# Performance work log

Measured on AMD Instinct MI355X. Metric: run time of the kernel, lower is better.

## Reference

```python
import jax, jax.numpy as jnp
import numpy as np

B, S, D, E, TOP_K = 2, 1024, 1024, 8, 2
H = 4 * D  # FFN hidden


def setup_inputs() -> dict:
    key = jax.random.key(0)
    ks = jax.random.split(key, 12)
    sc = 0.02
    return {
        "x": jax.random.normal(ks[0], (B, S, D), jnp.float32),
        # gate: nn.Linear(D, E) -> weight [E, D], bias [E]; routing bias param [E]
        "Wg": jax.random.normal(ks[1], (E, D), jnp.float32) * sc,
        "bg": jnp.zeros((E,), jnp.float32),
        "bias": jnp.zeros((E,), jnp.float32),
        # routed experts: stacked Linear(D,4D) and Linear(4D,D) weights (torch layout [out,in])
        "W1": jax.random.normal(ks[2], (E, H, D), jnp.float32) * sc,
        "b1": jnp.zeros((E, H), jnp.float32),
        "W2": jax.random.normal(ks[3], (E, D, H), jnp.float32) * sc,
        "b2": jnp.zeros((E, D), jnp.float32),
        # shared expert
        "Ws1": jax.random.normal(ks[4], (H, D), jnp.float32) * sc,
        "bs1": jnp.zeros((H,), jnp.float32),
        "Ws2": jax.random.normal(ks[5], (D, H), jnp.float32) * sc,
        "bs2": jnp.zeros((D,), jnp.float32),
    }


def reference(x, Wg, bg, bias, W1, b1, W2, b2, Ws1, bs1, Ws2, bs2):
    b, s, d = x.shape
    xf = x.reshape(-1, d)  # [T, D]
    T = xf.shape[0]

    # sigmoid gating with learnable routing bias
    scores = jax.nn.sigmoid(xf @ Wg.T + bg + bias)          # [T, E]
    top_scores, top_idx = jax.lax.top_k(scores, TOP_K)      # [T, K]

    # per-token per-expert combine weights (zero for unselected experts)
    weights = jnp.zeros((T, E), scores.dtype)
    weights = weights.at[jnp.arange(T)[:, None], top_idx].add(top_scores)  # [T, E]

    # dense grouped expert MLP (mask-and-matmul form of gather-GEMM-scatter)
    h = jax.nn.gelu(jnp.einsum("td,ehd->teh", xf, W1) + b1, approximate=False)  # [T, E, H]
    eo = jnp.einsum("teh,edh->ted", h, W2) + b2                                  # [T, E, D]
    combined = jnp.einsum("ted,te->td", eo, weights)                             # [T, D]

    # shared expert applied to every token
    shared = jax.nn.gelu(xf @ Ws1.T + bs1, approximate=False) @ Ws2.T + bs2      # [T, D]

    return (shared + combined).reshape(b, s, d)
```

## Files before the change

kernel.cpp:

```cpp
#include <hip/hip_runtime.h>
#include <hip/hip_bf16.h>
#include <math.h>

#define NTOK 2048
#define DDIM 1024
#define HDIM 4096
#define NEXP 8
#define NROWS (3 * NTOK)
#define KSPLIT2 2

typedef __bf16 bf16x8 __attribute__((ext_vector_type(8)));
typedef float f32x4 __attribute__((ext_vector_type(4)));
typedef __attribute__((address_space(1))) char as1_char;
typedef __attribute__((address_space(3))) char as3_char;

__device__ __forceinline__ void async16(const void* g, void* l) {
  __builtin_amdgcn_global_load_lds((as1_char*)g, (as3_char*)l, 16, 0, 0);
}

__device__ __forceinline__ float gelu_fast(float v) {
  const float x = v * 0.70710678118654752f;
  const float ax = fabsf(x);
  const float t = __builtin_amdgcn_rcpf(1.0f + 0.3275911f * ax);
  float p = 1.061405429f;
  p = p * t - 1.453152027f;
  p = p * t + 1.421413741f;
  p = p * t - 0.284496736f;
  p = p * t + 0.254829592f;
  const float y = 1.0f - p * t * __expf(-ax * ax);
  const float erfv = copysignf(y, x);
  return 0.5f * v * (1.0f + erfv);
}

__global__ void moe_zero_misc(int* counts) {
  if (threadIdx.x < NEXP) counts[threadIdx.x] = 0;
}

__device__ __forceinline__ void cvt2048(const float* __restrict__ src,
                                        __hip_bfloat16* __restrict__ dst,
                                        int tid) {
  const size_t i = (size_t)tid * 8;
  const float4 a = *(const float4*)(src + i);
  const float4 b = *(const float4*)(src + i + 4);
  union { __hip_bfloat16 h[8]; uint4 u; } p;
  p.h[0] = __float2bfloat16(a.x); p.h[1] = __float2bfloat16(a.y);
  p.h[2] = __float2bfloat16(a.z); p.h[3] = __float2bfloat16(a.w);
  p.h[4] = __float2bfloat16(b.x); p.h[5] = __float2bfloat16(b.y);
  p.h[6] = __float2bfloat16(b.z); p.h[7] = __float2bfloat16(b.w);
  *(uint4*)(dst + i) = p.u;
}

__global__ void __launch_bounds__(256) moe_pre(
    const float* __restrict__ x, const float* __restrict__ Wg,
    const float* __restrict__ bg, const float* __restrict__ bias,
    const float* __restrict__ W1, const float* __restrict__ Ws1,
    __hip_bfloat16* __restrict__ xbf, __hip_bfloat16* __restrict__ W1bf,
    __hip_bfloat16* __restrict__ Ws1bf, float* __restrict__ out,
    int* __restrict__ counts, int* __restrict__ topk_idx,
    float* __restrict__ topk_w, int* __restrict__ slot) {
  const int b = blockIdx.x, tid = threadIdx.x;
  if (b < 512) {
    const int t = b * 4 + (tid >> 6);
    const int lane = tid & 63;
    float xv[16];
#pragma unroll
    for (int q = 0; q < 16; ++q) xv[q] = x[(size_t)t * DDIM + q * 64 + lane];
    float sc[NEXP];
#pragma unroll
    for (int e = 0; e < NEXP; ++e) {
      float s = 0.f;
#pragma unroll
      for (int q = 0; q < 16; ++q) s += xv[q] * Wg[(size_t)e * DDIM + q * 64 + lane];
#pragma unroll
      for (int o = 32; o > 0; o >>= 1) s += __shfl_xor(s, o, 64);
      sc[e] = 1.0f / (1.0f + expf(-(s + bg[e] + bias[e])));
    }
    if (lane == 0) {
      int k0 = 0;
      for (int e = 1; e < NEXP; ++e)
        if (sc[e] > sc[k0]) k0 = e;
      int k1 = (k0 == 0) ? 1 : 0;
      for (int e = 0; e < NEXP; ++e) {
        if (e == k0) continue;
        if (sc[e] > sc[k1]) k1 = e;
      }
      topk_idx[t * 2 + 0] = k0;
      topk_idx[t * 2 + 1] = k1;
      topk_w[t * 2 + 0] = sc[k0];
      topk_w[t * 2 + 1] = sc[k1];
      slot[t * 2 + 0] = atomicAdd(&counts[k0], 1);
      slot[t * 2 + 1] = atomicAdd(&counts[k1], 1);
    }
    return;
  }
  const int cb = b - 512;
  if (cb < 1024) { cvt2048(x + (size_t)cb * 2048, xbf + (size_t)cb * 2048, tid); return; }
  if (cb < 17408) { const size_t o = (size_t)(cb - 1024) * 2048; cvt2048(W1 + o, W1bf + o, tid); return; }
  if (cb < 19456) { const size_t o = (size_t)(cb - 17408) * 2048; cvt2048(Ws1 + o, Ws1bf + o, tid); return; }
  const size_t o = (size_t)(cb - 19456) * 2048 + (size_t)tid * 8;
  *(float4*)(out + o) = make_float4(0.f, 0.f, 0.f, 0.f);
  *(float4*)(out + o + 4) = make_float4(0.f, 0.f, 0.f, 0.f);
}

__device__ __forceinline__ void gemm_core(const char* ga0, const char* ga1,
                                          const char* gb0, const char* gb1,
                                          char* sm, int Kbytes, int tid,
                                          f32x4 acc[4][4]) {
  const int w = tid >> 6, l = tid & 63;
  const int lr = l & 15, quad = l >> 4;
  const int wr = w >> 1, wc = w & 1;
  const int swz = (lr >> 1) & 3;
  const int aoff = (wr * 64 + lr) * 64 + ((quad ^ swz) * 16);
  const int boff = 8192 + (wc * 64 + lr) * 64 + ((quad ^ swz) * 16);
  const int niter = Kbytes >> 6;

  auto stage = [&](int it, int buf) {
    char* base = sm + buf * 16384 + w * 1024;
    const int kb = it * 64;
    async16(ga0 + kb, base);
    async16(ga1 + kb, base + 4096);
    async16(gb0 + kb, base + 8192);
    async16(gb1 + kb, base + 12288);
  };

  stage(0, 0);
  __builtin_amdgcn_s_waitcnt(0x0F70);
  __builtin_amdgcn_s_barrier();
  for (int i = 0; i < niter; ++i) {
    const int cur = i & 1;
    const bool more = (i + 1 < niter);
    if (more) stage(i + 1, cur ^ 1);
    const char* rb = sm + cur * 16384;
    bf16x8 av[4], bv[4];
#pragma unroll
    for (int i2 = 0; i2 < 4; ++i2) av[i2] = *(const bf16x8*)(rb + aoff + i2 * 1024);
#pragma unroll
    for (int j = 0; j < 4; ++j) bv[j] = *(const bf16x8*)(rb + boff + j * 1024);
#pragma unroll
    for (int i2 = 0; i2 < 4; ++i2)
#pragma unroll
      for (int j = 0; j < 4; ++j)
        acc[i2][j] = __builtin_amdgcn_mfma_f32_16x16x32_bf16(av[i2], bv[j], acc[i2][j], 0, 0, 0);
    if (more) {
      __builtin_amdgcn_s_waitcnt(0x0F70);
      __builtin_amdgcn_s_barrier();
    }
  }
}

__device__ __forceinline__ int stage_colb(int l) {
  return (((l & 3) ^ ((l >> 3) & 3)) * 16);
}

__device__ __forceinline__ void xcd_decode(int hw, int& g, int& m) {
  m = (hw >> 3) & 7;
  g = (hw & 7) + 8 * (hw >> 6);
}

__global__ void moe_scan(const int* __restrict__ counts, int* __restrict__ offsets) {
  if (threadIdx.x == 0) {
    int s = 0;
    for (int e = 0; e < NEXP; ++e) { offsets[e] = s; s += counts[e]; }
    offsets[NEXP] = s;
  }
}

__global__ void moe_scatter(const int* __restrict__ topk_idx, const float* __restrict__ topk_w,
                            const int* __restrict__ slot, const int* __restrict__ offsets,
                            int* __restrict__ row_token, float* __restrict__ row_w) {
  const int t = blockIdx.x * blockDim.x + threadIdx.x;
  if (t >= NTOK) return;
#pragma unroll
  for (int k = 0; k < 2; ++k) {
    const int e = topk_idx[t * 2 + k];
    const int rg = offsets[e] + slot[t * 2 + k];
    row_token[rg] = t;
    row_w[rg] = topk_w[t * 2 + k];
  }
  row_token[2 * NTOK + t] = t;
  row_w[2 * NTOK + t] = 1.0f;
}

__device__ __forceinline__ void cvt_w2_quota(int b, const float* __restrict__ W2,
                                             const float* __restrict__ Ws2,
                                             __hip_bfloat16* __restrict__ W2bf,
                                             __hip_bfloat16* __restrict__ Ws2bf,
                                             int tid) {
  const float* src;
  __hip_bfloat16* dst;
  size_t base;
  if (b < 4096) { src = W2; dst = W2bf; base = (size_t)b * 8192; }
  else          { src = Ws2; dst = Ws2bf; base = (size_t)(b - 4096) * 8192; }
#pragma unroll
  for (int k = 0; k < 8; ++k) {
    const size_t i = base + (size_t)k * 1024 + (size_t)tid * 4;
    const float4 a = *(const float4*)(src + i);
    union { __hip_bfloat16 h[4]; uint2 u; } p;
    p.h[0] = __float2bfloat16(a.x); p.h[1] = __float2bfloat16(a.y);
    p.h[2] = __float2bfloat16(a.z); p.h[3] = __float2bfloat16(a.w);
    *(uint2*)(dst + i) = p.u;
  }
}

__global__ void __launch_bounds__(256) moe_gemm1(
    const __hip_bfloat16* __restrict__ xbf, const __hip_bfloat16* __restrict__ W1bf,
    const float* __restrict__ b1, const __hip_bfloat16* __restrict__ Ws1bf,
    const float* __restrict__ bs1, const int* __restrict__ counts,
    const int* __restrict__ offsets, const int* __restrict__ row_token,
    __hip_bfloat16* __restrict__ h1, const float* __restrict__ W2,
    const float* __restrict__ Ws2, __hip_bfloat16* __restrict__ W2bf,
    __hip_bfloat16* __restrict__ Ws2bf) {
  __shared__ alignas(16) char sm[32768];
  const int tid = threadIdx.x;
  int g, m;
  xcd_decode(blockIdx.x, g, m);
  const int nt = m + 8 * (g & 3);
  const int mt = (g >> 2) & 15;
  const int e = g >> 6;
  const int cnt = (e < NEXP) ? counts[e] : NTOK;
  if (mt * 128 >= cnt) {
    cvt_w2_quota(blockIdx.x, W2, Ws2, W2bf, Ws2bf, tid);
    return;
  }
  const int off = (e < NEXP) ? offsets[e] : 2 * NTOK;
  const __hip_bfloat16* Bw = (e < NEXP) ? (W1bf + (size_t)e * HDIM * DDIM) : Ws1bf;
  const float* bb = (e < NEXP) ? (b1 + e * HDIM) : bs1;

  const int w = tid >> 6, l = tid & 63;
  const int mrow = w * 16 + (l >> 2);
  const int colb = stage_colb(l);

  const int r0 = mt * 128 + mrow, r1 = r0 + 64;
  const int c0 = (r0 < cnt) ? r0 : (cnt - 1);
  const int c1 = (r1 < cnt) ? r1 : (cnt - 1);
  const int t0 = row_token[off + c0];
  const int t1 = row_token[off + c1];
  const char* ga0 = (const char*)xbf + (size_t)t0 * (DDIM * 2) + colb;
  const char* ga1 = (const char*)xbf + (size_t)t1 * (DDIM * 2) + colb;
  const char* gb0 = (const char*)Bw + (size_t)(nt * 128 + mrow) * (DDIM * 2) + colb;
  const char* gb1 = (const char*)Bw + (size_t)(nt * 128 + mrow + 64) * (DDIM * 2) + colb;

  f32x4 acc[4][4] = {};
  gemm_core(ga0, ga1, gb0, gb1, sm, DDIM * 2, tid, acc);

  const int lr = l & 15, quad = l >> 4, wr = w >> 1, wc = w & 1;
#pragma unroll
  for (int i = 0; i < 4; ++i) {
#pragma unroll
    for (int r = 0; r < 4; ++r) {
      const int rowe = mt * 128 + wr * 64 + i * 16 + quad * 4 + r;
      if (rowe >= cnt) continue;
      const size_t orow = (size_t)(off + rowe) * HDIM;
#pragma unroll
      for (int j = 0; j < 4; ++j) {
        const int h = nt * 128 + wc * 64 + j * 16 + lr;
        const float v = acc[i][j][r] + bb[h];
        h1[orow + h] = __float2bfloat16(gelu_fast(v));
      }
    }
  }
  cvt_w2_quota(blockIdx.x, W2, Ws2, W2bf, Ws2bf, tid);
}

__global__ void __launch_bounds__(256) moe_gemm2(
    const __hip_bfloat16* __restrict__ h1, const __hip_bfloat16* __restrict__ W2bf,
    const float* __restrict__ b2, const __hip_bfloat16* __restrict__ Ws2bf,
    const float* __restrict__ bs2, const int* __restrict__ counts,
    const int* __restrict__ offsets, const int* __restrict__ row_token,
    const float* __restrict__ row_w, float* __restrict__ out) {
  __shared__ alignas(16) char sm[32768];
  int g, m;
  xcd_decode(blockIdx.x, g, m);
  const int nt = m;
  const int kc = g & 1;
  const int mt = (g >> 1) & 15;
  const int e = g >> 5;
  const int cnt = (e < NEXP) ? counts[e] : NTOK;
  if (mt * 128 >= cnt) return;
  const int off = (e < NEXP) ? offsets[e] : 2 * NTOK;
  const __hip_bfloat16* Bw = (e < NEXP) ? (W2bf + (size_t)e * DDIM * HDIM) : Ws2bf;
  const float* bb = (e < NEXP) ? (b2 + e * DDIM) : bs2;

  const int tid = threadIdx.x;
  const int w = tid >> 6, l = tid & 63;
  const int mrow = w * 16 + (l >> 2);
  const int colb = stage_colb(l);
  const int KB = (HDIM * 2) / KSPLIT2;
  const size_t kofs = (size_t)kc * KB;

  const char* ga0 = (const char*)h1 + (size_t)(off + mt * 128 + mrow) * (HDIM * 2) + kofs + colb;
  const char* ga1 = (const char*)h1 + (size_t)(off + mt * 128 + mrow + 64) * (HDIM * 2) + kofs + colb;
  const char* gb0 = (const char*)Bw + (size_t)(nt * 128 + mrow) * (HDIM * 2) + kofs + colb;
  const char* gb1 = (const char*)Bw + (size_t)(nt * 128 + mrow + 64) * (HDIM * 2) + kofs + colb;

  f32x4 acc[4][4] = {};
  gemm_core(ga0, ga1, gb0, gb1, sm, KB, tid, acc);

  const int lr = l & 15, quad = l >> 4, wr = w >> 1, wc = w & 1;
#pragma unroll
  for (int i = 0; i < 4; ++i) {
#pragma unroll
    for (int r = 0; r < 4; ++r) {
      const int rowe = mt * 128 + wr * 64 + i * 16 + quad * 4 + r;
      if (rowe >= cnt) continue;
      const int rg = off + rowe;
      const int tok = row_token[rg];
      const float wt = row_w[rg];
#pragma unroll
      for (int j = 0; j < 4; ++j) {
        const int d = nt * 128 + wc * 64 + j * 16 + lr;
        const float base = (kc == 0) ? bb[d] : 0.f;
        atomicAdd(&out[(size_t)tok * DDIM + d], wt * (acc[i][j][r] + base));
      }
    }
  }
}

extern "C" void kernel_launch(void* const* d_in, const int* in_sizes, int n_in,
                              void* d_out, int out_size, void* d_ws, size_t ws_size,
                              hipStream_t stream) {
  (void)in_sizes; (void)n_in; (void)out_size; (void)ws_size;
  const float* x    = (const float*)d_in[0];
  const float* Wg   = (const float*)d_in[1];
  const float* bg   = (const float*)d_in[2];
  const float* bias = (const float*)d_in[3];
  const float* W1   = (const float*)d_in[4];
  const float* b1   = (const float*)d_in[5];
  const float* W2   = (const float*)d_in[6];
  const float* b2   = (const float*)d_in[7];
  const float* Ws1  = (const float*)d_in[8];
  const float* bs1  = (const float*)d_in[9];
  const float* Ws2  = (const float*)d_in[10];
  const float* bs2  = (const float*)d_in[11];
  float* out = (float*)d_out;

  char* ws = (char*)d_ws;
  size_t cur = 0;
  auto take = [&](size_t b) -> void* {
    void* p = ws + cur;
    cur += (b + 255) & ~(size_t)255;
    return p;
  };
  int* counts    = (int*)take(NEXP * 4);
  int* offsets   = (int*)take((NEXP + 1) * 4);
  int* topk_idx  = (int*)take(NTOK * 2 * 4);
  float* topk_w  = (float*)take(NTOK * 2 * 4);
  int* slot      = (int*)take(NTOK * 2 * 4);
  int* row_token = (int*)take(NROWS * 4);
  float* row_w   = (float*)take(NROWS * 4);
  __hip_bfloat16* xbf   = (__hip_bfloat16*)take((size_t)NTOK * DDIM * 2);
  __hip_bfloat16* W1bf  = (__hip_bfloat16*)take((size_t)NEXP * HDIM * DDIM * 2);
  __hip_bfloat16* W2bf  = (__hip_bfloat16*)take((size_t)NEXP * DDIM * HDIM * 2);
  __hip_bfloat16* Ws1bf = (__hip_bfloat16*)take((size_t)HDIM * DDIM * 2);
  __hip_bfloat16* Ws2bf = (__hip_bfloat16*)take((size_t)DDIM * HDIM * 2);
  __hip_bfloat16* h1    = (__hip_bfloat16*)take((size_t)(NROWS + 64) * HDIM * 2);

  moe_zero_misc<<<1, 64, 0, stream>>>(counts);

  moe_pre<<<20992, 256, 0, stream>>>(x, Wg, bg, bias, W1, Ws1,
                                     xbf, W1bf, Ws1bf, out,
                                     counts, topk_idx, topk_w, slot);

  moe_scan<<<1, 1, 0, stream>>>(counts, offsets);
  moe_scatter<<<NTOK / 256, 256, 0, stream>>>(topk_idx, topk_w, slot, offsets, row_token, row_w);

  moe_gemm1<<<4608, 256, 0, stream>>>(xbf, W1bf, b1, Ws1bf, bs1, counts, offsets,
                                      row_token, h1, W2, Ws2, W2bf, Ws2bf);

  moe_gemm2<<<2304, 256, 0, stream>>>(h1, W2bf, b2, Ws2bf, bs2, counts, offsets,
                                      row_token, row_w, out);
}
```

Baseline: 362.5 us.

## Double K-tile depth to 128 bytes with 8-way XOR swizzle and deeper prefetch

The shared GEMM core now stages a 64-element K slice per iteration instead of 32, using 64KB of LDS double buffering, an 8-slot XOR swizzle and four row pointers per operand. It waits only for the older batch of async loads (partial vmcnt) before the barrier, so the next tile's loads stay in flight during compute, and it issues twice as many MFMAs per barrier. The aim is to halve barrier and loop overhead and hide global-to-LDS latency better. The cost is doubled LDS per block, which may cut occupancy, plus an extra barrier per iteration.

Result: faster. 328.2 us (-9.5%).

```diff
diff --git a/kernel.cpp b/kernel.cpp
--- a/kernel.cpp
+++ b/kernel.cpp
@@ -102,54 +102,60 @@
   *(float4*)(out + o + 4) = make_float4(0.f, 0.f, 0.f, 0.f);
 }
 
-__device__ __forceinline__ void gemm_core(const char* ga0, const char* ga1,
-                                          const char* gb0, const char* gb1,
+__device__ __forceinline__ void gemm_core(const char* const ga[4], const char* const gb[4],
                                           char* sm, int Kbytes, int tid,
                                           f32x4 acc[4][4]) {
   const int w = tid >> 6, l = tid & 63;
   const int lr = l & 15, quad = l >> 4;
   const int wr = w >> 1, wc = w & 1;
-  const int swz = (lr >> 1) & 3;
-  const int aoff = (wr * 64 + lr) * 64 + ((quad ^ swz) * 16);
-  const int boff = 8192 + (wc * 64 + lr) * 64 + ((quad ^ swz) * 16);
-  const int niter = Kbytes >> 6;
+  const int s8 = lr & 7;
+  const int slot0 = (quad ^ s8) * 16;
+  const int slot1 = ((4 + quad) ^ s8) * 16;
+  const int abase = (wr * 64 + lr) * 128;
+  const int bbase = 16384 + (wc * 64 + lr) * 128;
+  const int niter = Kbytes >> 7;
 
   auto stage = [&](int it, int buf) {
-    char* base = sm + buf * 16384 + w * 1024;
-    const int kb = it * 64;
-    async16(ga0 + kb, base);
-    async16(ga1 + kb, base + 4096);
-    async16(gb0 + kb, base + 8192);
-    async16(gb1 + kb, base + 12288);
+    char* base = sm + buf * 32768;
+    const int kb = it * 128;
+#pragma unroll
+    for (int q = 0; q < 4; ++q) {
+      async16(ga[q] + kb, base + w * 4096 + q * 1024);
+      async16(gb[q] + kb, base + 16384 + w * 4096 + q * 1024);
+    }
   };
 
   stage(0, 0);
-  __builtin_amdgcn_s_waitcnt(0x0F70);
-  __builtin_amdgcn_s_barrier();
   for (int i = 0; i < niter; ++i) {
     const int cur = i & 1;
-    const bool more = (i + 1 < niter);
-    if (more) stage(i + 1, cur ^ 1);
-    const char* rb = sm + cur * 16384;
-    bf16x8 av[4], bv[4];
-#pragma unroll
-    for (int i2 = 0; i2 < 4; ++i2) av[i2] = *(const bf16x8*)(rb + aoff + i2 * 1024);
-#pragma unroll
-    for (int j = 0; j < 4; ++j) bv[j] = *(const bf16x8*)(rb + boff + j * 1024);
-#pragma unroll
-    for (int i2 = 0; i2 < 4; ++i2)
-#pragma unroll
-      for (int j = 0; j < 4; ++j)
-        acc[i2][j] = __builtin_amdgcn_mfma_f32_16x16x32_bf16(av[i2], bv[j], acc[i2][j], 0, 0, 0);
-    if (more) {
+    if (i + 1 < niter) {
+      stage(i + 1, cur ^ 1);
+      __builtin_amdgcn_s_waitcnt(0x0F78);
+    } else {
       __builtin_amdgcn_s_waitcnt(0x0F70);
-      __builtin_amdgcn_s_barrier();
-    }
-  }
-}
-
-__device__ __forceinline__ int stage_colb(int l) {
-  return (((l & 3) ^ ((l >> 3) & 3)) * 16);
+    }
+    __builtin_amdgcn_s_barrier();
+    const char* rb = sm + cur * 32768;
+    bf16x8 av[4][2], bv[4][2];
+#pragma unroll
+    for (int i2 = 0; i2 < 4; ++i2) {
+      av[i2][0] = *(const bf16x8*)(rb + abase + i2 * 2048 + slot0);
+      av[i2][1] = *(const bf16x8*)(rb + abase + i2 * 2048 + slot1);
+    }
+#pragma unroll
+    for (int j = 0; j < 4; ++j) {
+      bv[j][0] = *(const bf16x8*)(rb + bbase + j * 2048 + slot0);
+      bv[j][1] = *(const bf16x8*)(rb + bbase + j * 2048 + slot1);
+    }
+#pragma unroll
+    for (int s = 0; s < 2; ++s)
+#pragma unroll
+      for (int i2 = 0; i2 < 4; ++i2)
+#pragma unroll
+        for (int j = 0; j < 4; ++j)
+          acc[i2][j] = __builtin_amdgcn_mfma_f32_16x16x32_bf16(av[i2][s], bv[j][s], acc[i2][j], 0, 0, 0);
+    __builtin_amdgcn_s_barrier();
+  }
 }
 
 __device__ __forceinline__ void xcd_decode(int hw, int& g, int& m) {
@@ -210,7 +216,7 @@
     __hip_bfloat16* __restrict__ h1, const float* __restrict__ W2,
     const float* __restrict__ Ws2, __hip_bfloat16* __restrict__ W2bf,
     __hip_bfloat16* __restrict__ Ws2bf) {
-  __shared__ alignas(16) char sm[32768];
+  __shared__ alignas(16) char sm[65536];
   const int tid = threadIdx.x;
   int g, m;
   xcd_decode(blockIdx.x, g, m);
@@ -227,21 +233,22 @@
   const float* bb = (e < NEXP) ? (b1 + e * HDIM) : bs1;
 
   const int w = tid >> 6, l = tid & 63;
-  const int mrow = w * 16 + (l >> 2);
-  const int colb = stage_colb(l);
-
-  const int r0 = mt * 128 + mrow, r1 = r0 + 64;
-  const int c0 = (r0 < cnt) ? r0 : (cnt - 1);
-  const int c1 = (r1 < cnt) ? r1 : (cnt - 1);
-  const int t0 = row_token[off + c0];
-  const int t1 = row_token[off + c1];
-  const char* ga0 = (const char*)xbf + (size_t)t0 * (DDIM * 2) + colb;
-  const char* ga1 = (const char*)xbf + (size_t)t1 * (DDIM * 2) + colb;
-  const char* gb0 = (const char*)Bw + (size_t)(nt * 128 + mrow) * (DDIM * 2) + colb;
-  const char* gb1 = (const char*)Bw + (size_t)(nt * 128 + mrow + 64) * (DDIM * 2) + colb;
+  const int rl8 = l >> 3;
+  const int cg = ((l & 7) ^ rl8) * 16;
+
+  const char* ga[4];
+  const char* gb[4];
+#pragma unroll
+  for (int q = 0; q < 4; ++q) {
+    const int r = mt * 128 + w * 32 + q * 8 + rl8;
+    const int c = (r < cnt) ? r : (cnt - 1);
+    const int tok = row_token[off + c];
+    ga[q] = (const char*)xbf + (size_t)tok * (DDIM * 2) + cg;
+    gb[q] = (const char*)Bw + (size_t)(nt * 128 + w * 32 + q * 8 + rl8) * (DDIM * 2) + cg;
+  }
 
   f32x4 acc[4][4] = {};
-  gemm_core(ga0, ga1, gb0, gb1, sm, DDIM * 2, tid, acc);
+  gemm_core(ga, gb, sm, DDIM * 2, tid, acc);
 
   const int lr = l & 15, quad = l >> 4, wr = w >> 1, wc = w & 1;
 #pragma unroll
@@ -268,7 +275,7 @@
     const float* __restrict__ bs2, const int* __restrict__ counts,
     const int* __restrict__ offsets, const int* __restrict__ row_token,
     const float* __restrict__ row_w, float* __restrict__ out) {
-  __shared__ alignas(16) char sm[32768];
+  __shared__ alignas(16) char sm[65536];
   int g, m;
   xcd_decode(blockIdx.x, g, m);
   const int nt = m;
@@ -283,18 +290,22 @@
 
   const int tid = threadIdx.x;
   const int w = tid >> 6, l = tid & 63;
-  const int mrow = w * 16 + (l >> 2);
-  const int colb = stage_colb(l);
+  const int rl8 = l >> 3;
+  const int cg = ((l & 7) ^ rl8) * 16;
   const int KB = (HDIM * 2) / KSPLIT2;
   const size_t kofs = (size_t)kc * KB;
 
-  const char* ga0 = (const char*)h1 + (size_t)(off + mt * 128 + mrow) * (HDIM * 2) + kofs + colb;
-  const char* ga1 = (const char*)h1 + (size_t)(off + mt * 128 + mrow + 64) * (HDIM * 2) + kofs + colb;
-  const char* gb0 = (const char*)Bw + (size_t)(nt * 128 + mrow) * (HDIM * 2) + kofs + colb;
-  const char* gb1 = (const char*)Bw + (size_t)(nt * 128 + mrow + 64) * (HDIM * 2) + kofs + colb;
+  const char* ga[4];
+  const char* gb[4];
+#pragma unroll
+  for (int q = 0; q < 4; ++q) {
+    const int ar = mt * 128 + w * 32 + q * 8 + rl8;
+    ga[q] = (const char*)h1 + (size_t)(off + ar) * (HDIM * 2) + kofs + cg;
+    gb[q] = (const char*)Bw + (size_t)(nt * 128 + w * 32 + q * 8 + rl8) * (HDIM * 2) + kofs + cg;
+  }
 
   f32x4 acc[4][4] = {};
-  gemm_core(ga0, ga1, gb0, gb1, sm, KB, tid, acc);
+  gemm_core(ga, gb, sm, KB, tid, acc);
 
   const int lr = l & 15, quad = l >> 4, wr = w >> 1, wc = w & 1;
 #pragma unroll
```
